# Kernel tuning notes

Measured on AMD Instinct MI355X. Metric: run time of the kernel, lower is better.

Reference implementation:

```python
import jax, jax.numpy as jnp
import numpy as np

PS = 32
EMBED_DIM = 768
IN_CH = 3
IMG = 1024
NUM_PATCHES = 992  # ini_row = i for H=1024, so need i+32 <= 1024
SPIKE_IDX = np.array([5, 300, 800])
SPIKE_VAL = 1.0e6  # makes val ~= 23.94 < 24 -> nearest size 16 -> subdivided


def _token_layout(iw_np, num_patches, ps, H):
    """Replicates the module's data-dependent patch-size / subpatch-position logic.
    Returns static (rows, cols, sizes) for every output token, in emission order."""
    avg = iw_np.mean()
    val = np.minimum(ps * avg ** 0.05 / iw_np ** 0.05, float(ps))
    choices = np.array([32, 16, 8, 4], dtype=np.float64)  # argmin picks first on tie, like min(list)
    sizes = choices[np.argmin(np.abs(val[:, None] - choices[None, :]), axis=1)].astype(np.int64)
    rows, cols, szs = [], [], []
    for i in range(num_patches):
        ini_col = (i * ps) % H
        ini_row = (i * ps * ps) // H
        s = int(sizes[i])
        if 3 < s < ps:
            ns = ps // s  # num_subpatches; subpatch_size == s
            for j in range(ns):
                rows.append(ini_row + (j * s) // ns)
                cols.append(ini_col + (j * s) % (ns * s))
                szs.append(s)
        else:
            rows.append(ini_row)
            cols.append(ini_col)
            szs.append(ps)
    return np.asarray(rows), np.asarray(cols), np.asarray(szs)


def _embed(x, W, b, rows, cols, szs, ps):
    E, C = W.shape[0], W.shape[1]
    B = x.shape[0]
    T = szs.shape[0]
    out = jnp.zeros((B, T, E), dtype=x.dtype)
    for s in np.unique(szs):
        s = int(s)
        idx = np.nonzero(szs == s)[0]  # static token slots for this size group
        r, c = rows[idx], cols[idx]
        if s == ps:
            Wf = W
        else:
            kd = ps // s  # fold the ps x ps kernel down to s x s, as in the module
            Wf = W.reshape(E, C, kd, kd, s, s).sum(axis=(2, 3))
        ar = np.arange(s)
        # gather [B, C, K, s, s] sub-patches with static advanced indexing
        patches = x[:, :, r[:, None, None] + ar[None, :, None], c[:, None, None] + ar[None, None, :]]
        tok = jnp.einsum('bckhw,echw->bke', patches, Wf) + b  # stride==kernel -> 1 token each
        out = out.at[:, jnp.asarray(idx), :].set(tok)
    return out


def setup_inputs() -> dict:
    key = jax.random.key(0)
    k_x, k_w, k_iw, k_b = jax.random.split(key, 4)
    x = jax.random.normal(k_x, (8, IN_CH, IMG, IMG), dtype=jnp.float32)
    iw = jax.random.uniform(k_iw, (1, NUM_PATCHES), dtype=jnp.float32, minval=0.5, maxval=1.5)
    iw = iw.at[0, SPIKE_IDX].set(SPIKE_VAL)  # 3 high-importance patches -> size-16 subdivision
    W = jax.random.normal(k_w, (EMBED_DIM, IN_CH, PS, PS), dtype=jnp.float32) * 0.02
    b = jax.random.normal(k_b, (EMBED_DIM,), dtype=jnp.float32) * 0.02
    return {"x": x, "importance_weights": iw, "W": W, "b": b, "num_patches": NUM_PATCHES}


def reference(x, importance_weights, W, b, num_patches):
    iw = np.asarray(importance_weights)[0]
    rows, cols, szs = _token_layout(iw, int(num_patches), PS, x.shape[3])
    return _embed(x, W, b, rows, cols, szs, PS)  # [B, T, E]
```

## Files before the change

kernel.cpp:

```cpp
#include <hip/hip_runtime.h>


typedef __attribute__((ext_vector_type(8))) short bf16x8;
typedef __attribute__((ext_vector_type(4))) float f32x4;

#define K_DIM 3072
#define N_DIM 768

__device__ __forceinline__ unsigned short f2bf(float f) {
  unsigned int u = __float_as_uint(f);
  u += 0x7fffu + ((u >> 16) & 1u);
  return (unsigned short)(u >> 16);
}

__global__ __launch_bounds__(1024)
void prep_kernel(const float* __restrict__ W, unsigned short* __restrict__ Wb, int w4,
                 const float* __restrict__ iw, int P,
                 int* __restrict__ tokBase, int* __restrict__ tokMask, int NB_W) {
  int bid = blockIdx.x;
  int tid = threadIdx.x;
  if (bid < NB_W) {
    int idx = bid * 1024 + tid;
    if (idx < w4) {
      float4 f = *(const float4*)(W + (size_t)idx * 4);
      ushort4 o;
      o.x = f2bf(f.x); o.y = f2bf(f.y); o.z = f2bf(f.z); o.w = f2bf(f.w);
      *(ushort4*)(Wb + (size_t)idx * 4) = o;
    }
    return;
  }
  __shared__ double s_wsum[16];
  __shared__ double s_avg;
  __shared__ int s_cnt[1024];
  float v = (tid < P) ? iw[tid] : 0.0f;
  double d = (double)v;
#pragma unroll
  for (int off = 32; off > 0; off >>= 1) d += __shfl_down(d, off, 64);
  if ((tid & 63) == 0) s_wsum[tid >> 6] = d;
  __syncthreads();
  if (tid == 0) {
    double s = 0.0;
    for (int i = 0; i < 16; ++i) s += s_wsum[i];
    s_avg = s / (double)P;
  }
  __syncthreads();
  int cnt = 0, sz = 32;
  if (tid < P) {
    double val = 32.0 * pow(s_avg / (double)v, 0.05);
    if (val > 32.0) val = 32.0;
    sz = (val >= 24.0) ? 32 : (val >= 12.0) ? 16 : (val >= 6.0) ? 8 : 4;
    cnt = (sz < 32) ? (32 / sz) : 1;
  }
  s_cnt[tid] = cnt;
  __syncthreads();
  for (int dl = 1; dl < 1024; dl <<= 1) {
    int add = (tid >= dl) ? s_cnt[tid - dl] : 0;
    __syncthreads();
    s_cnt[tid] += add;
    __syncthreads();
  }
  if (tid < P) {
    int off = s_cnt[tid] - cnt;
    int ini_col = (tid * 32) & 1023;
    int ini_row = (tid * 32 * 32) >> 10;
    if (sz == 32) {
      tokBase[off] = ini_row * 1024 + ini_col;
      tokMask[off] = 31;
    } else {
      int ns = 32 / sz;
      for (int j = 0; j < ns; ++j) {
        int r = ini_row + (j * sz) / ns;
        int c = ini_col + ((j * sz) & 31);
        tokBase[off + j] = r * 1024 + c;
        tokMask[off + j] = sz - 1;
      }
    }
  }
}

__global__ __launch_bounds__(256)
void gather_kernel(const float* __restrict__ x,
                   const int* __restrict__ tokBase,
                   const int* __restrict__ tokMask,
                   unsigned short* __restrict__ Ab) {
  int t = blockIdx.x;
  int b = blockIdx.y;
  int T = gridDim.x;
  int m = b * T + t;
  int base = tokBase[t];
  int mask = tokMask[t];
  int sh = __popc(mask);
  const float* xb = x + (size_t)b * 3145728 + (size_t)base;
  unsigned short* arow = Ab + (size_t)m * K_DIM;
#pragma unroll
  for (int it = 0; it < 3; ++it) {
    int g = it * 256 + threadIdx.x;
    int p = g * 4;
    int c = p >> 10;
    int f = p & 1023;
    int h = (f >> sh) & mask;
    int w = f & mask;
    float4 fv = *(const float4*)(xb + (size_t)c * 1048576 + h * 1024 + w);
    ushort4 o;
    o.x = f2bf(fv.x); o.y = f2bf(fv.y); o.z = f2bf(fv.z); o.w = f2bf(fv.w);
    *(ushort4*)(arow + p) = o;
  }
}

__global__ __launch_bounds__(256, 2)
void gemm_kernel(const unsigned short* __restrict__ A, const unsigned short* __restrict__ Wb,
                 const float* __restrict__ bias, float* __restrict__ out, int Mtot) {
  __shared__ unsigned short Alds[128 * 32];
  __shared__ unsigned short Blds[128 * 32];
  int tid = threadIdx.x;
  int lane = tid & 63;
  int wave = tid >> 6;
  int wr = wave >> 1, wc = wave & 1;
  int mBase = blockIdx.y * 128;
  int nBase = blockIdx.x * 128;

  f32x4 acc[4][4] = {};

  const unsigned short* Ag0 = A + (size_t)(mBase + (tid >> 2)) * K_DIM + (tid & 3) * 8;
  const unsigned short* Ag1 = Ag0 + (size_t)64 * K_DIM;
  const unsigned short* Bg0 = Wb + (size_t)(nBase + (tid >> 2)) * K_DIM + (tid & 3) * 8;
  const unsigned short* Bg1 = Bg0 + (size_t)64 * K_DIM;
  unsigned short* Al0 = Alds + tid * 8;
  unsigned short* Al1 = Al0 + 2048;
  unsigned short* Bl0 = Blds + tid * 8;
  unsigned short* Bl1 = Bl0 + 2048;

  int rr = lane & 15, q = lane >> 4;

  int4 ra0, ra1, rb0, rb1;
  int4 sa0, sa1, sb0, sb1;

  ra0 = *(const int4*)(Ag0); ra1 = *(const int4*)(Ag1);
  rb0 = *(const int4*)(Bg0); rb1 = *(const int4*)(Bg1);

#define MFMA_STAGE()                                                        \
  {                                                                         \
    bf16x8 aF[4], bF[4];                                                    \
    _Pragma("unroll")                                                       \
    for (int i = 0; i < 4; ++i)                                             \
      aF[i] = *(const bf16x8*)&Alds[(wr * 64 + i * 16 + rr) * 32 + q * 8];  \
    _Pragma("unroll")                                                       \
    for (int j = 0; j < 4; ++j)                                             \
      bF[j] = *(const bf16x8*)&Blds[(wc * 64 + j * 16 + rr) * 32 + q * 8];  \
    _Pragma("unroll")                                                       \
    for (int i = 0; i < 4; ++i)                                             \
      _Pragma("unroll")                                                     \
      for (int j = 0; j < 4; ++j)                                           \
        acc[i][j] = __builtin_amdgcn_mfma_f32_16x16x32_bf16(aF[i], bF[j],   \
                                                            acc[i][j], 0, 0, 0); \
  }

  for (int k0 = 0; k0 < K_DIM; k0 += 64) {
    if (k0 + 32 < K_DIM) {
      sa0 = *(const int4*)(Ag0 + k0 + 32); sa1 = *(const int4*)(Ag1 + k0 + 32);
      sb0 = *(const int4*)(Bg0 + k0 + 32); sb1 = *(const int4*)(Bg1 + k0 + 32);
    }
    __syncthreads();
    *(int4*)Al0 = ra0; *(int4*)Al1 = ra1;
    *(int4*)Bl0 = rb0; *(int4*)Bl1 = rb1;
    __syncthreads();
    MFMA_STAGE();

    if (k0 + 64 < K_DIM) {
      ra0 = *(const int4*)(Ag0 + k0 + 64); ra1 = *(const int4*)(Ag1 + k0 + 64);
      rb0 = *(const int4*)(Bg0 + k0 + 64); rb1 = *(const int4*)(Bg1 + k0 + 64);
    }
    __syncthreads();
    *(int4*)Al0 = sa0; *(int4*)Al1 = sa1;
    *(int4*)Bl0 = sb0; *(int4*)Bl1 = sb1;
    __syncthreads();
    MFMA_STAGE();
  }

#pragma unroll
  for (int j = 0; j < 4; ++j) {
    int n = nBase + wc * 64 + j * 16 + rr;
    float bv = bias[n];
#pragma unroll
    for (int i = 0; i < 4; ++i) {
      int mrow = mBase + wr * 64 + i * 16 + q * 4;
#pragma unroll
      for (int r2 = 0; r2 < 4; ++r2) {
        int m = mrow + r2;
        if (m < Mtot) out[(size_t)m * N_DIM + n] = acc[i][j][r2] + bv;
      }
    }
  }
}

extern "C" void kernel_launch(void* const* d_in, const int* in_sizes, int n_in,
                              void* d_out, int out_size, void* d_ws, size_t ws_size,
                              hipStream_t stream) {
  const float* x  = (const float*)d_in[0];
  const float* iw = (const float*)d_in[1];
  const float* W  = (const float*)d_in[2];
  const float* b  = (const float*)d_in[3];
  int P = in_sizes[1];
  int B = in_sizes[0] / (3 * 1024 * 1024);
  int E = in_sizes[3];
  int T = out_size / (B * E);
  int Mtot = B * T;
  int Mpad = (Mtot + 127) & ~127;

  char* ws = (char*)d_ws;
  int* tokBase = (int*)ws;
  int* tokMask = (int*)(ws + 32768);
  unsigned short* Wb = (unsigned short*)(ws + 65536);
  unsigned short* Ab = (unsigned short*)(ws + 65536 + (size_t)E * K_DIM * 2);

  int w4 = E * K_DIM / 4;
  int NB_W = (w4 + 1023) / 1024;
  prep_kernel<<<NB_W + 1, 1024, 0, stream>>>(W, Wb, w4, iw, P, tokBase, tokMask, NB_W);

  dim3 gGrid(T, B);
  gather_kernel<<<gGrid, 256, 0, stream>>>(x, tokBase, tokMask, Ab);

  dim3 grid(N_DIM / 128, Mpad / 128);
  gemm_kernel<<<grid, 256, 0, stream>>>(Ab, Wb, b, (float*)d_out, Mtot);
}
```

Measured before the change: 262.2 us.

## Use direct global-to-LDS loads with double-buffered swizzled tiles in GEMM

The GEMM main loop now stages A and B tiles straight into LDS with global_load_lds, skipping the register round-trip. It uses two LDS buffers holding K=64 tiles and an XOR swizzle on the 16-byte chunks to avoid bank conflicts. This removes one of the two barrier pairs per iteration and overlaps the next tile's load with the current MFMA work. LDS use grows to 64KB per block, which may limit occupancy under the 2-blocks-per-CU launch bound. Correctness depends on the direct loads having completed by the single barrier.

```diff
diff --git a/kernel.cpp b/kernel.cpp
--- a/kernel.cpp
+++ b/kernel.cpp
@@ -11,6 +11,12 @@
   unsigned int u = __float_as_uint(f);
   u += 0x7fffu + ((u >> 16) & 1u);
   return (unsigned short)(u >> 16);
+}
+
+__device__ __forceinline__ void gload16(const void* g, void* l) {
+  __builtin_amdgcn_global_load_lds(
+      (const __attribute__((address_space(1))) void*)g,
+      (__attribute__((address_space(3))) void*)l, 16, 0, 0);
 }
 
 __global__ __launch_bounds__(1024)
@@ -110,8 +116,7 @@
 __global__ __launch_bounds__(256, 2)
 void gemm_kernel(const unsigned short* __restrict__ A, const unsigned short* __restrict__ Wb,
                  const float* __restrict__ bias, float* __restrict__ out, int Mtot) {
-  __shared__ unsigned short Alds[128 * 32];
-  __shared__ unsigned short Blds[128 * 32];
+  __shared__ unsigned short lds[2][2][128 * 64];
   int tid = threadIdx.x;
   int lane = tid & 63;
   int wave = tid >> 6;
@@ -121,61 +126,64 @@
 
   f32x4 acc[4][4] = {};
 
-  const unsigned short* Ag0 = A + (size_t)(mBase + (tid >> 2)) * K_DIM + (tid & 3) * 8;
-  const unsigned short* Ag1 = Ag0 + (size_t)64 * K_DIM;
-  const unsigned short* Bg0 = Wb + (size_t)(nBase + (tid >> 2)) * K_DIM + (tid & 3) * 8;
-  const unsigned short* Bg1 = Bg0 + (size_t)64 * K_DIM;
-  unsigned short* Al0 = Alds + tid * 8;
-  unsigned short* Al1 = Al0 + 2048;
-  unsigned short* Bl0 = Blds + tid * 8;
-  unsigned short* Bl1 = Bl0 + 2048;
+  int lrow = lane >> 3;
+  int schunk = (lane & 7) ^ lrow;
+  const unsigned short* Ag = A + (size_t)(mBase + wave * 32 + lrow) * K_DIM + schunk * 8;
+  const unsigned short* Bg = Wb + (size_t)(nBase + wave * 32 + lrow) * K_DIM + schunk * 8;
+  unsigned short* Adst0 = &lds[0][0][(wave * 32) * 64] + lane * 8;
+  unsigned short* Bdst0 = &lds[0][1][(wave * 32) * 64] + lane * 8;
+
+#define STAGE(BUF, KOFF)                                                    \
+  {                                                                         \
+    _Pragma("unroll")                                                       \
+    for (int inst = 0; inst < 4; ++inst) {                                  \
+      gload16(Ag + (size_t)(inst * 8) * K_DIM + (KOFF),                     \
+              Adst0 + (size_t)(BUF) * 2 * 8192 + inst * 512);               \
+      gload16(Bg + (size_t)(inst * 8) * K_DIM + (KOFF),                     \
+              Bdst0 + (size_t)(BUF) * 2 * 8192 + inst * 512);               \
+    }                                                                       \
+  }
 
   int rr = lane & 15, q = lane >> 4;
-
-  int4 ra0, ra1, rb0, rb1;
-  int4 sa0, sa1, sb0, sb1;
-
-  ra0 = *(const int4*)(Ag0); ra1 = *(const int4*)(Ag1);
-  rb0 = *(const int4*)(Bg0); rb1 = *(const int4*)(Bg1);
-
-#define MFMA_STAGE()                                                        \
+  int r7 = rr & 7;
+
+#define COMPUTE(BUF)                                                        \
   {                                                                         \
-    bf16x8 aF[4], bF[4];                                                    \
+    const unsigned short* Ab_ = &lds[BUF][0][0];                            \
+    const unsigned short* Bb_ = &lds[BUF][1][0];                            \
     _Pragma("unroll")                                                       \
-    for (int i = 0; i < 4; ++i)                                             \
-      aF[i] = *(const bf16x8*)&Alds[(wr * 64 + i * 16 + rr) * 32 + q * 8];  \
-    _Pragma("unroll")                                                       \
-    for (int j = 0; j < 4; ++j)                                             \
-      bF[j] = *(const bf16x8*)&Blds[(wc * 64 + j * 16 + rr) * 32 + q * 8];  \
-    _Pragma("unroll")                                                       \
-    for (int i = 0; i < 4; ++i)                                             \
+    for (int kh = 0; kh < 2; ++kh) {                                        \
+      bf16x8 aF[4], bF[4];                                                  \
+      _Pragma("unroll")                                                     \
+      for (int i = 0; i < 4; ++i)                                           \
+        aF[i] = *(const bf16x8*)&Ab_[(wr * 64 + i * 16 + rr) * 64 +         \
+                                     ((kh * 4 + q) ^ r7) * 8];              \
       _Pragma("unroll")                                                     \
       for (int j = 0; j < 4; ++j)                                           \
-        acc[i][j] = __builtin_amdgcn_mfma_f32_16x16x32_bf16(aF[i], bF[j],   \
-                                                            acc[i][j], 0, 0, 0); \
-  }
-
+        bF[j] = *(const bf16x8*)&Bb_[(wc * 64 + j * 16 + rr) * 64 +         \
+                                     ((kh * 4 + q) ^ r7) * 8];              \
+      _Pragma("unroll")                                                     \
+      for (int i = 0; i < 4; ++i)                                           \
+        _Pragma("unroll")                                                   \
+        for (int j = 0; j < 4; ++j)                                         \
+          acc[i][j] = __builtin_amdgcn_mfma_f32_16x16x32_bf16(aF[i], bF[j], \
+                                                              acc[i][j], 0, 0, 0); \
+    }                                                                       \
+  }
+
+  STAGE(0, 0)
+  __syncthreads();
+  int buf = 0;
   for (int k0 = 0; k0 < K_DIM; k0 += 64) {
-    if (k0 + 32 < K_DIM) {
-      sa0 = *(const int4*)(Ag0 + k0 + 32); sa1 = *(const int4*)(Ag1 + k0 + 32);
-      sb0 = *(const int4*)(Bg0 + k0 + 32); sb1 = *(const int4*)(Bg1 + k0 + 32);
-    }
+    if (k0 + 64 < K_DIM) {
+      if (buf == 0) STAGE(1, k0 + 64) else STAGE(0, k0 + 64)
+    }
+    if (buf == 0) COMPUTE(0) else COMPUTE(1)
     __syncthreads();
-    *(int4*)Al0 = ra0; *(int4*)Al1 = ra1;
-    *(int4*)Bl0 = rb0; *(int4*)Bl1 = rb1;
-    __syncthreads();
-    MFMA_STAGE();
-
-    if (k0 + 64 < K_DIM) {
-      ra0 = *(const int4*)(Ag0 + k0 + 64); ra1 = *(const int4*)(Ag1 + k0 + 64);
-      rb0 = *(const int4*)(Bg0 + k0 + 64); rb1 = *(const int4*)(Bg1 + k0 + 64);
-    }
-    __syncthreads();
-    *(int4*)Al0 = sa0; *(int4*)Al1 = sa1;
-    *(int4*)Bl0 = sb0; *(int4*)Bl1 = sb1;
-    __syncthreads();
-    MFMA_STAGE();
-  }
+    buf ^= 1;
+  }
+#undef STAGE
+#undef COMPUTE
 
 #pragma unroll
   for (int j = 0; j < 4; ++j) {
@@ -220,6 +228,7 @@
   dim3 gGrid(T, B);
   gather_kernel<<<gGrid, 256, 0, stream>>>(x, tokBase, tokMask, Ab);
 
+
   dim3 grid(N_DIM / 128, Mpad / 128);
   gemm_kernel<<<grid, 256, 0, stream>>>(Ab, Wb, b, (float*)d_out, Mtot);
 }
```

Result: faster. 246.3 us (-6.1%).
